# Kernel tuning notes

Hardware: AMD Instinct MI355X
Metric: run time of the kernel (lower is better)

Reference implementation:

```python
import jax, jax.numpy as jnp
import numpy as np

S = 2048          # sequence length == max_seq_len
B = 256           # input_bits per token
H = 8             # num voting heads
NPER = 12         # RAM bits per neuron: min(similarity_bits, 12)
NPOS = 11         # relative-position bits: ceil(log2(max_seq_len))
SIM = 2 * B + NPOS  # similarity input bits = [query | key | rel_dist]
THRESH = H // 2   # threshold aggregation cutoff
MAXD = S - 1


def setup_inputs() -> dict:
    key = jax.random.key(0)
    k1, k2, k3 = jax.random.split(key, 3)
    tokens = jax.random.randint(k1, (S, B), 0, 2).astype(jnp.int32)      # bit tokens
    conn = jax.random.randint(k2, (H, NPER), 0, SIM).astype(jnp.int32)   # RAM wiring per head
    table = jax.random.randint(k3, (H, 2 ** NPER), 0, 2).astype(jnp.int32)  # RAM contents (0/1)
    return {"tokens": tokens, "conn": conn, "table": table}


def reference(tokens, conn, table):
    powers = (1 << jnp.arange(NPER)).astype(jnp.int32)            # address bit weights
    q_mask = (conn < B).astype(jnp.int32)
    k_mask = ((conn >= B) & (conn < 2 * B)).astype(jnp.int32)
    p_mask = (conn >= 2 * B).astype(jnp.int32)

    # Address decomposes additively over the three concat regions since wiring is fixed.
    tq = jnp.take(tokens, jnp.clip(conn, 0, B - 1), axis=1)        # [S,H,NPER]
    q_contrib = jnp.sum(tq * (q_mask * powers)[None], axis=-1)     # [S,H]
    tk = jnp.take(tokens, jnp.clip(conn - B, 0, B - 1), axis=1)
    k_contrib = jnp.sum(tk * (k_mask * powers)[None], axis=-1)     # [S,H]

    d = jnp.arange(S)
    rel_bits = ((d[:, None] >> jnp.arange(NPOS)[None, :]) & 1).astype(jnp.int32)  # [S,NPOS]
    tp = jnp.take(rel_bits, jnp.clip(conn - 2 * B, 0, NPOS - 1), axis=1)          # [S,H,NPER]
    p_contrib = jnp.sum(tp * (p_mask * powers)[None], axis=-1)     # [S,H] indexed by distance

    i = jnp.arange(S)
    dist = jnp.clip(i[:, None] - i[None, :], 0, MAXD)              # [S,S]
    addr = q_contrib[:, None, :] + k_contrib[None, :, :] + p_contrib[dist]  # [S,S,H]
    head_bits = table[jnp.arange(H)[None, None, :], addr]          # [S,S,H] RAM lookups

    causal = i[None, :] <= i[:, None]
    votes = jnp.where(causal, head_bits.sum(-1), 0)                # [S,S]

    # threshold aggregation: XOR (per-bit parity) of tokens with vote >= THRESH
    include = (votes >= THRESH).astype(jnp.int32)                  # [S,S]
    parity = jnp.einsum('ij,jb->ib', include, tokens) % 2          # [S,B]
    # fallback: first token achieving the max vote when nothing clears threshold
    fallback = tokens[jnp.argmax(votes, axis=1)]                   # [S,B]
    any_included = include.sum(axis=1, keepdims=True) > 0
    out = jnp.where(any_included, parity, fallback)
    return out.astype(jnp.uint8)
```

## Files before the change

kernel.cpp:

```cpp
#include <hip/hip_runtime.h>
#include <stdint.h>

#define S 2048
#define B 256
#define THRESH 4

typedef unsigned long long u64;
typedef uint32_t u32;
typedef uint8_t u8;


__global__ void prep_kernel(const int* __restrict__ tokens,
                            const int* __restrict__ conn,
                            const int* __restrict__ table,
                            u64* __restrict__ ptok,
                            uint16_t* __restrict__ qc,
                            uint16_t* __restrict__ kc,
                            uint16_t* __restrict__ pc,
                            u8* __restrict__ tab8) {
    const int bi = blockIdx.x;
    const int tid = threadIdx.x;

    if (bi >= S) {
        const int base = (bi - S) * 1024 + tid * 4;
        const int4 v = *(const int4*)(table + base);
        uchar4 o;
        o.x = (u8)(v.x & 1); o.y = (u8)(v.y & 1);
        o.z = (u8)(v.z & 1); o.w = (u8)(v.w & 1);
        *(uchar4*)(tab8 + base) = o;
        return;
    }

    __shared__ u64 srow[4];
    const int i = bi;
    const int lane = tid & 63, wave = tid >> 6;

    const int t = tokens[i * B + tid];
    const u64 m = __ballot(t != 0);
    if (lane == 0) {
        srow[wave] = m;
        ptok[i * 4 + wave] = m;
    }
    __syncthreads();

    if (tid < 8) {
        const int h = tid;
        int q = 0, k = 0, p = 0;
        #pragma unroll
        for (int n = 0; n < 12; ++n) {
            const int c = conn[h * 12 + n];
            if (c < B) {
                q |= (int)((srow[c >> 6] >> (c & 63)) & 1) << n;
            } else if (c < 2 * B) {
                const int cc = c - B;
                k |= (int)((srow[cc >> 6] >> (cc & 63)) & 1) << n;
            } else {
                p |= ((i >> (c - 2 * B)) & 1) << n;
            }
        }
        qc[i * 8 + h] = (uint16_t)q;
        kc[i * 8 + h] = (uint16_t)k;
        pc[i * 8 + h] = (uint16_t)p;
    }
}

__device__ __forceinline__ int vote8(const u8* s_tab8, u64 a0, u64 a1) {
    const u32 lo0 = (u32)a0, hi0 = (u32)(a0 >> 32);
    const u32 lo1 = (u32)a1, hi1 = (u32)(a1 >> 32);
    int v;
    v  = s_tab8[          (lo0 & 0xFFF)];
    v += s_tab8[ 4096 + ((lo0 >> 16) & 0xFFF)];
    v += s_tab8[ 8192 +  (hi0 & 0xFFF)];
    v += s_tab8[12288 + ((hi0 >> 16) & 0xFFF)];
    v += s_tab8[16384 +  (lo1 & 0xFFF)];
    v += s_tab8[20480 + ((lo1 >> 16) & 0xFFF)];
    v += s_tab8[24576 +  (hi1 & 0xFFF)];
    v += s_tab8[28672 + ((hi1 >> 16) & 0xFFF)];
    return v;
}

__launch_bounds__(256)
__global__ void main_kernel(const u64* __restrict__ ptok,
                            const uint16_t* __restrict__ qc,
                            const uint16_t* __restrict__ kc,
                            const uint16_t* __restrict__ pc,
                            const u8* __restrict__ tab8,
                            int* __restrict__ out) {
    __shared__ u8  s_tab8[32768];
    __shared__ u64 s_part[8][256];
    __shared__ u64 s_p2[8][32];
    __shared__ u64 s_fin[8];
    __shared__ u64 s_kred[4];

    const int b   = blockIdx.x;
    const int tid = threadIdx.x;
    const int lane = tid & 63, wave = tid >> 6;

    #pragma unroll
    for (int k = 0; k < 8; ++k)
        ((uint4*)s_tab8)[tid + k * 256] = ((const uint4*)tab8)[tid + k * 256];
    __syncthreads();

    const int rowA = (b == 1023) ? 2047 : 2046 - b;
    const int rowB = (b == 1023) ? 1023 : b;
    const int nA    = rowA + 1;
    const int total = nA + rowB + 1;
    const int niter = total >> 9;

    const ulonglong2 qA = *(const ulonglong2*)(qc + rowA * 8);
    const ulonglong2 qB = *(const ulonglong2*)(qc + rowB * 8);

    u64 ax0=0, ax1=0, ax2=0, ax3=0;
    u64 bx0=0, bx1=0, bx2=0, bx3=0;
    u32 bkA = 2047u, bkB = 2047u;

    for (int it = 0; it < niter; ++it) {
        const int v0 = (it << 9) + tid;
        const int v1 = v0 + 256;

        const bool isA0 = (v0 < nA);
        const bool isA1 = (v1 < nA);
        const int j0 = isA0 ? v0 : v0 - nA;
        const int j1 = isA1 ? v1 : v1 - nA;
        const int d0 = (isA0 ? rowA : rowB) - j0;
        const int d1 = (isA1 ? rowA : rowB) - j1;

        const ulonglong2 kk0 = *(const ulonglong2*)(kc + j0 * 8);
        const ulonglong2 pp0 = *(const ulonglong2*)(pc + d0 * 8);
        const ulonglong2 t00 = *(const ulonglong2*)(ptok + j0 * 4);
        const ulonglong2 t01 = *(const ulonglong2*)(ptok + j0 * 4 + 2);
        const ulonglong2 kk1 = *(const ulonglong2*)(kc + j1 * 8);
        const ulonglong2 pp1 = *(const ulonglong2*)(pc + d1 * 8);
        const ulonglong2 t10 = *(const ulonglong2*)(ptok + j1 * 4);
        const ulonglong2 t11 = *(const ulonglong2*)(ptok + j1 * 4 + 2);

        const int vt0 = vote8(s_tab8, (isA0 ? qA.x : qB.x) + kk0.x + pp0.x,
                                      (isA0 ? qA.y : qB.y) + kk0.y + pp0.y);
        const int vt1 = vote8(s_tab8, (isA1 ? qA.x : qB.x) + kk1.x + pp1.x,
                                      (isA1 ? qA.y : qB.y) + kk1.y + pp1.y);

        const u32 vk0 = ((u32)(vt0 + 1) << 16) | (u32)(2047 - j0);
        const u32 vk1 = ((u32)(vt1 + 1) << 16) | (u32)(2047 - j1);

        if (isA0) { if (vk0 > bkA) bkA = vk0; } else { if (vk0 > bkB) bkB = vk0; }
        if (isA1) { if (vk1 > bkA) bkA = vk1; } else { if (vk1 > bkB) bkB = vk1; }

        if (vt0 >= THRESH) {
            if (isA0) { ax0 ^= t00.x; ax1 ^= t00.y; ax2 ^= t01.x; ax3 ^= t01.y; }
            else      { bx0 ^= t00.x; bx1 ^= t00.y; bx2 ^= t01.x; bx3 ^= t01.y; }
        }
        if (vt1 >= THRESH) {
            if (isA1) { ax0 ^= t10.x; ax1 ^= t10.y; ax2 ^= t11.x; ax3 ^= t11.y; }
            else      { bx0 ^= t10.x; bx1 ^= t10.y; bx2 ^= t11.x; bx3 ^= t11.y; }
        }
    }

    #pragma unroll
    for (int off = 32; off; off >>= 1) {
        bkA = max(bkA, (u32)__shfl_xor((int)bkA, off));
        bkB = max(bkB, (u32)__shfl_xor((int)bkB, off));
    }

    s_part[0][tid] = ax0; s_part[1][tid] = ax1; s_part[2][tid] = ax2; s_part[3][tid] = ax3;
    s_part[4][tid] = bx0; s_part[5][tid] = bx1; s_part[6][tid] = bx2; s_part[7][tid] = bx3;
    if (lane == 0) s_kred[wave] = ((u64)bkA << 32) | bkB;
    __syncthreads();

    {
        const int w = tid >> 5, c = tid & 31;
        u64 x = s_part[w][c]       ^ s_part[w][c + 32]  ^ s_part[w][c + 64]  ^ s_part[w][c + 96]
              ^ s_part[w][c + 128] ^ s_part[w][c + 160] ^ s_part[w][c + 192] ^ s_part[w][c + 224];
        s_p2[w][c] = x;
    }
    __syncthreads();
    if (tid < 64) {
        const int w = tid >> 3, c = tid & 7;
        u64 x = s_p2[w][c] ^ s_p2[w][c + 8] ^ s_p2[w][c + 16] ^ s_p2[w][c + 24];
        x ^= __shfl_xor(x, 4); x ^= __shfl_xor(x, 2); x ^= __shfl_xor(x, 1);
        if (c == 0) s_fin[w] = x;
    }
    __syncthreads();

    const u32 fkA = max(max((u32)(s_kred[0] >> 32), (u32)(s_kred[1] >> 32)),
                        max((u32)(s_kred[2] >> 32), (u32)(s_kred[3] >> 32)));
    const u32 fkB = max(max((u32)s_kred[0], (u32)s_kred[1]),
                        max((u32)s_kred[2], (u32)s_kred[3]));

    const int widx = tid >> 6, bitb = tid & 63;
    int oA, oB;
    if ((fkA >> 16) > THRESH) {
        oA = (int)((s_fin[widx] >> bitb) & 1);
    } else {
        const int bj = 2047 - (int)(fkA & 0xFFFF);
        oA = (int)((ptok[bj * 4 + widx] >> bitb) & 1);
    }
    if ((fkB >> 16) > THRESH) {
        oB = (int)((s_fin[4 + widx] >> bitb) & 1);
    } else {
        const int bj = 2047 - (int)(fkB & 0xFFFF);
        oB = (int)((ptok[bj * 4 + widx] >> bitb) & 1);
    }
    out[rowA * B + tid] = oA;
    out[rowB * B + tid] = oB;
}

extern "C" void kernel_launch(void* const* d_in, const int* in_sizes, int n_in,
                              void* d_out, int out_size, void* d_ws, size_t ws_size,
                              hipStream_t stream) {
    const int* tokens = (const int*)d_in[0];
    const int* conn   = (const int*)d_in[1];
    const int* table  = (const int*)d_in[2];
    int* outp = (int*)d_out;

    uint8_t* ws = (uint8_t*)d_ws;
    u64*      ptok = (u64*)(ws);
    uint16_t* qcp  = (uint16_t*)(ws + 65536);
    uint16_t* kcp  = (uint16_t*)(ws + 98304);
    uint16_t* pcp  = (uint16_t*)(ws + 131072);
    u8*       tab8 = (u8*)(ws + 163840);

    prep_kernel<<<S + 32, 256, 0, stream>>>(tokens, conn, table, ptok, qcp, kcp, pcp, tab8);
    main_kernel<<<S / 2, 256, 0, stream>>>(ptok, qcp, kcp, pcp, tab8, outp);
}
```

Before: 23.15 us.

## Bit-pack RAM tables into u32 words and batch 8 rows per prep block

Measured after the change: 19.83 us. 1.17x faster.

```diff
diff --git a/kernel.cpp b/kernel.cpp
--- a/kernel.cpp
+++ b/kernel.cpp
@@ -7,7 +7,6 @@
 
 typedef unsigned long long u64;
 typedef uint32_t u32;
-typedef uint8_t u8;
 
 
 __global__ void prep_kernel(const int* __restrict__ tokens,
@@ -17,43 +16,46 @@
                             uint16_t* __restrict__ qc,
                             uint16_t* __restrict__ kc,
                             uint16_t* __restrict__ pc,
-                            u8* __restrict__ tab8) {
-    const int bi = blockIdx.x;
-    const int tid = threadIdx.x;
-
-    if (bi >= S) {
-        const int base = (bi - S) * 1024 + tid * 4;
-        const int4 v = *(const int4*)(table + base);
-        uchar4 o;
-        o.x = (u8)(v.x & 1); o.y = (u8)(v.y & 1);
-        o.z = (u8)(v.z & 1); o.w = (u8)(v.w & 1);
-        *(uchar4*)(tab8 + base) = o;
+                            u32* __restrict__ ptab) {
+    const int bi = blockIdx.x, tid = threadIdx.x;
+
+    if (bi >= 256) {
+        const int m = (bi - 256) * 256 + tid;
+        const int* src = table + m * 32;
+        u32 v = 0;
+        #pragma unroll
+        for (int b = 0; b < 32; ++b) v |= (u32)(src[b] & 1) << b;
+        ptab[m] = v;
         return;
     }
 
-    __shared__ u64 srow[4];
-    const int i = bi;
+    __shared__ u32 s_conn[96];
+    __shared__ u64 s_row[8][4];
     const int lane = tid & 63, wave = tid >> 6;
 
-    const int t = tokens[i * B + tid];
-    const u64 m = __ballot(t != 0);
-    if (lane == 0) {
-        srow[wave] = m;
-        ptok[i * 4 + wave] = m;
-    }
-    __syncthreads();
-
-    if (tid < 8) {
-        const int h = tid;
+    if (tid < 96) s_conn[tid] = (u32)conn[tid];
+
+    const int r0 = bi * 8;
+    #pragma unroll
+    for (int r = 0; r < 8; ++r) {
+        const int t = tokens[(r0 + r) * B + tid];
+        const u64 m = __ballot(t != 0);
+        if (lane == 0) { s_row[r][wave] = m; ptok[(r0 + r) * 4 + wave] = m; }
+    }
+    __syncthreads();
+
+    if (tid < 64) {
+        const int r = tid >> 3, h = tid & 7;
+        const int i = r0 + r;
         int q = 0, k = 0, p = 0;
         #pragma unroll
         for (int n = 0; n < 12; ++n) {
-            const int c = conn[h * 12 + n];
+            const int c = (int)s_conn[h * 12 + n];
             if (c < B) {
-                q |= (int)((srow[c >> 6] >> (c & 63)) & 1) << n;
+                q |= (int)((s_row[r][c >> 6] >> (c & 63)) & 1) << n;
             } else if (c < 2 * B) {
                 const int cc = c - B;
-                k |= (int)((srow[cc >> 6] >> (cc & 63)) & 1) << n;
+                k |= (int)((s_row[r][cc >> 6] >> (cc & 63)) & 1) << n;
             } else {
                 p |= ((i >> (c - 2 * B)) & 1) << n;
             }
@@ -64,18 +66,15 @@
     }
 }
 
-__device__ __forceinline__ int vote8(const u8* s_tab8, u64 a0, u64 a1) {
-    const u32 lo0 = (u32)a0, hi0 = (u32)(a0 >> 32);
-    const u32 lo1 = (u32)a1, hi1 = (u32)(a1 >> 32);
-    int v;
-    v  = s_tab8[          (lo0 & 0xFFF)];
-    v += s_tab8[ 4096 + ((lo0 >> 16) & 0xFFF)];
-    v += s_tab8[ 8192 +  (hi0 & 0xFFF)];
-    v += s_tab8[12288 + ((hi0 >> 16) & 0xFFF)];
-    v += s_tab8[16384 +  (lo1 & 0xFFF)];
-    v += s_tab8[20480 + ((lo1 >> 16) & 0xFFF)];
-    v += s_tab8[24576 +  (hi1 & 0xFFF)];
-    v += s_tab8[28672 + ((hi1 >> 16) & 0xFFF)];
+__device__ __forceinline__ int vote8(const u32* s_tab, u64 a0, u64 a1) {
+    int v = 0;
+    #pragma unroll
+    for (int h = 0; h < 4; ++h) {
+        { u32 w = (u32)(a0 >> (16 * h + 5)) & 127;
+          v += (int)((s_tab[h * 128 + w] >> ((u32)(a0 >> (16 * h)) & 31)) & 1); }
+        { u32 w = (u32)(a1 >> (16 * h + 5)) & 127;
+          v += (int)((s_tab[(h + 4) * 128 + w] >> ((u32)(a1 >> (16 * h)) & 31)) & 1); }
+    }
     return v;
 }
 
@@ -84,9 +83,9 @@
                             const uint16_t* __restrict__ qc,
                             const uint16_t* __restrict__ kc,
                             const uint16_t* __restrict__ pc,
-                            const u8* __restrict__ tab8,
+                            const u32* __restrict__ ptab,
                             int* __restrict__ out) {
-    __shared__ u8  s_tab8[32768];
+    __shared__ u32 s_tab[1024];
     __shared__ u64 s_part[8][256];
     __shared__ u64 s_p2[8][32];
     __shared__ u64 s_fin[8];
@@ -96,9 +95,7 @@
     const int tid = threadIdx.x;
     const int lane = tid & 63, wave = tid >> 6;
 
-    #pragma unroll
-    for (int k = 0; k < 8; ++k)
-        ((uint4*)s_tab8)[tid + k * 256] = ((const uint4*)tab8)[tid + k * 256];
+    ((uint4*)s_tab)[tid] = ((const uint4*)ptab)[tid];
     __syncthreads();
 
     const int rowA = (b == 1023) ? 2047 : 2046 - b;
@@ -134,10 +131,10 @@
         const ulonglong2 t10 = *(const ulonglong2*)(ptok + j1 * 4);
         const ulonglong2 t11 = *(const ulonglong2*)(ptok + j1 * 4 + 2);
 
-        const int vt0 = vote8(s_tab8, (isA0 ? qA.x : qB.x) + kk0.x + pp0.x,
-                                      (isA0 ? qA.y : qB.y) + kk0.y + pp0.y);
-        const int vt1 = vote8(s_tab8, (isA1 ? qA.x : qB.x) + kk1.x + pp1.x,
-                                      (isA1 ? qA.y : qB.y) + kk1.y + pp1.y);
+        const int vt0 = vote8(s_tab, (isA0 ? qA.x : qB.x) + kk0.x + pp0.x,
+                                     (isA0 ? qA.y : qB.y) + kk0.y + pp0.y);
+        const int vt1 = vote8(s_tab, (isA1 ? qA.x : qB.x) + kk1.x + pp1.x,
+                                     (isA1 ? qA.y : qB.y) + kk1.y + pp1.y);
 
         const u32 vk0 = ((u32)(vt0 + 1) << 16) | (u32)(2047 - j0);
         const u32 vk1 = ((u32)(vt1 + 1) << 16) | (u32)(2047 - j1);
@@ -217,8 +214,8 @@
     uint16_t* qcp  = (uint16_t*)(ws + 65536);
     uint16_t* kcp  = (uint16_t*)(ws + 98304);
     uint16_t* pcp  = (uint16_t*)(ws + 131072);
-    u8*       tab8 = (u8*)(ws + 163840);
-
-    prep_kernel<<<S + 32, 256, 0, stream>>>(tokens, conn, table, ptok, qcp, kcp, pcp, tab8);
-    main_kernel<<<S / 2, 256, 0, stream>>>(ptok, qcp, kcp, pcp, tab8, outp);
-}
+    u32*      ptab = (u32*)(ws + 163840);
+
+    prep_kernel<<<260, 256, 0, stream>>>(tokens, conn, table, ptok, qcp, kcp, pcp, ptab);
+    main_kernel<<<S / 2, 256, 0, stream>>>(ptok, qcp, kcp, pcp, ptab, outp);
+}
```

## Batch prep rows per block and alias reduction buffer onto table LDS

Applied to the files above, without the earlier changes.

New measurement: 20.87 us. -9.9%, faster.

```diff
diff --git a/kernel.cpp b/kernel.cpp
--- a/kernel.cpp
+++ b/kernel.cpp
@@ -18,11 +18,10 @@
                             uint16_t* __restrict__ kc,
                             uint16_t* __restrict__ pc,
                             u8* __restrict__ tab8) {
-    const int bi = blockIdx.x;
-    const int tid = threadIdx.x;
-
-    if (bi >= S) {
-        const int base = (bi - S) * 1024 + tid * 4;
+    const int bi = blockIdx.x, tid = threadIdx.x;
+
+    if (bi >= 256) {
+        const int base = (bi - 256) * 1024 + tid * 4;
         const int4 v = *(const int4*)(table + base);
         uchar4 o;
         o.x = (u8)(v.x & 1); o.y = (u8)(v.y & 1);
@@ -31,29 +30,33 @@
         return;
     }
 
-    __shared__ u64 srow[4];
-    const int i = bi;
+    __shared__ u32 s_conn[96];
+    __shared__ u64 s_row[8][4];
     const int lane = tid & 63, wave = tid >> 6;
 
-    const int t = tokens[i * B + tid];
-    const u64 m = __ballot(t != 0);
-    if (lane == 0) {
-        srow[wave] = m;
-        ptok[i * 4 + wave] = m;
-    }
-    __syncthreads();
-
-    if (tid < 8) {
-        const int h = tid;
+    if (tid < 96) s_conn[tid] = (u32)conn[tid];
+
+    const int r0 = bi * 8;
+    #pragma unroll
+    for (int r = 0; r < 8; ++r) {
+        const int t = tokens[(r0 + r) * B + tid];
+        const u64 m = __ballot(t != 0);
+        if (lane == 0) { s_row[r][wave] = m; ptok[(r0 + r) * 4 + wave] = m; }
+    }
+    __syncthreads();
+
+    if (tid < 64) {
+        const int r = tid >> 3, h = tid & 7;
+        const int i = r0 + r;
         int q = 0, k = 0, p = 0;
         #pragma unroll
         for (int n = 0; n < 12; ++n) {
-            const int c = conn[h * 12 + n];
+            const int c = (int)s_conn[h * 12 + n];
             if (c < B) {
-                q |= (int)((srow[c >> 6] >> (c & 63)) & 1) << n;
+                q |= (int)((s_row[r][c >> 6] >> (c & 63)) & 1) << n;
             } else if (c < 2 * B) {
                 const int cc = c - B;
-                k |= (int)((srow[cc >> 6] >> (cc & 63)) & 1) << n;
+                k |= (int)((s_row[r][cc >> 6] >> (cc & 63)) & 1) << n;
             } else {
                 p |= ((i >> (c - 2 * B)) & 1) << n;
             }
@@ -86,11 +89,14 @@
                             const uint16_t* __restrict__ pc,
                             const u8* __restrict__ tab8,
                             int* __restrict__ out) {
-    __shared__ u8  s_tab8[32768];
-    __shared__ u64 s_part[8][256];
+    __shared__ __align__(16) u8 s_mem[32768];
     __shared__ u64 s_p2[8][32];
     __shared__ u64 s_fin[8];
     __shared__ u64 s_kred[4];
+
+    u8* s_tab8 = s_mem;
+    typedef u64 part_row[256];
+    part_row* s_part = reinterpret_cast<part_row*>(s_mem);
 
     const int b   = blockIdx.x;
     const int tid = threadIdx.x;
@@ -115,43 +121,28 @@
     u32 bkA = 2047u, bkB = 2047u;
 
     for (int it = 0; it < niter; ++it) {
-        const int v0 = (it << 9) + tid;
-        const int v1 = v0 + 256;
-
-        const bool isA0 = (v0 < nA);
-        const bool isA1 = (v1 < nA);
-        const int j0 = isA0 ? v0 : v0 - nA;
-        const int j1 = isA1 ? v1 : v1 - nA;
-        const int d0 = (isA0 ? rowA : rowB) - j0;
-        const int d1 = (isA1 ? rowA : rowB) - j1;
-
-        const ulonglong2 kk0 = *(const ulonglong2*)(kc + j0 * 8);
-        const ulonglong2 pp0 = *(const ulonglong2*)(pc + d0 * 8);
-        const ulonglong2 t00 = *(const ulonglong2*)(ptok + j0 * 4);
-        const ulonglong2 t01 = *(const ulonglong2*)(ptok + j0 * 4 + 2);
-        const ulonglong2 kk1 = *(const ulonglong2*)(kc + j1 * 8);
-        const ulonglong2 pp1 = *(const ulonglong2*)(pc + d1 * 8);
-        const ulonglong2 t10 = *(const ulonglong2*)(ptok + j1 * 4);
-        const ulonglong2 t11 = *(const ulonglong2*)(ptok + j1 * 4 + 2);
-
-        const int vt0 = vote8(s_tab8, (isA0 ? qA.x : qB.x) + kk0.x + pp0.x,
-                                      (isA0 ? qA.y : qB.y) + kk0.y + pp0.y);
-        const int vt1 = vote8(s_tab8, (isA1 ? qA.x : qB.x) + kk1.x + pp1.x,
-                                      (isA1 ? qA.y : qB.y) + kk1.y + pp1.y);
-
-        const u32 vk0 = ((u32)(vt0 + 1) << 16) | (u32)(2047 - j0);
-        const u32 vk1 = ((u32)(vt1 + 1) << 16) | (u32)(2047 - j1);
-
-        if (isA0) { if (vk0 > bkA) bkA = vk0; } else { if (vk0 > bkB) bkB = vk0; }
-        if (isA1) { if (vk1 > bkA) bkA = vk1; } else { if (vk1 > bkB) bkB = vk1; }
-
-        if (vt0 >= THRESH) {
-            if (isA0) { ax0 ^= t00.x; ax1 ^= t00.y; ax2 ^= t01.x; ax3 ^= t01.y; }
-            else      { bx0 ^= t00.x; bx1 ^= t00.y; bx2 ^= t01.x; bx3 ^= t01.y; }
-        }
-        if (vt1 >= THRESH) {
-            if (isA1) { ax0 ^= t10.x; ax1 ^= t10.y; ax2 ^= t11.x; ax3 ^= t11.y; }
-            else      { bx0 ^= t10.x; bx1 ^= t10.y; bx2 ^= t11.x; bx3 ^= t11.y; }
+        #pragma unroll
+        for (int s = 0; s < 2; ++s) {
+            const int v = (it << 9) + (s << 8) + tid;
+            const bool isA = (v < nA);
+            const int j = isA ? v : v - nA;
+            const int d = (isA ? rowA : rowB) - j;
+
+            const ulonglong2 kk = *(const ulonglong2*)(kc + j * 8);
+            const ulonglong2 pp = *(const ulonglong2*)(pc + d * 8);
+            const ulonglong2 t0 = *(const ulonglong2*)(ptok + j * 4);
+            const ulonglong2 t1 = *(const ulonglong2*)(ptok + j * 4 + 2);
+
+            const int vt = vote8(s_tab8, (isA ? qA.x : qB.x) + kk.x + pp.x,
+                                         (isA ? qA.y : qB.y) + kk.y + pp.y);
+
+            const u32 vk = ((u32)(vt + 1) << 16) | (u32)(2047 - j);
+            if (isA) { if (vk > bkA) bkA = vk; } else { if (vk > bkB) bkB = vk; }
+
+            if (vt >= THRESH) {
+                if (isA) { ax0 ^= t0.x; ax1 ^= t0.y; ax2 ^= t1.x; ax3 ^= t1.y; }
+                else     { bx0 ^= t0.x; bx1 ^= t0.y; bx2 ^= t1.x; bx3 ^= t1.y; }
+            }
         }
     }
 
@@ -161,6 +152,7 @@
         bkB = max(bkB, (u32)__shfl_xor((int)bkB, off));
     }
 
+    __syncthreads();
     s_part[0][tid] = ax0; s_part[1][tid] = ax1; s_part[2][tid] = ax2; s_part[3][tid] = ax3;
     s_part[4][tid] = bx0; s_part[5][tid] = bx1; s_part[6][tid] = bx2; s_part[7][tid] = bx3;
     if (lane == 0) s_kred[wave] = ((u64)bkA << 32) | bkB;
@@ -219,6 +211,6 @@
     uint16_t* pcp  = (uint16_t*)(ws + 131072);
     u8*       tab8 = (u8*)(ws + 163840);
 
-    prep_kernel<<<S + 32, 256, 0, stream>>>(tokens, conn, table, ptok, qcp, kcp, pcp, tab8);
+    prep_kernel<<<288, 256, 0, stream>>>(tokens, conn, table, ptok, qcp, kcp, pcp, tab8);
     main_kernel<<<S / 2, 256, 0, stream>>>(ptok, qcp, kcp, pcp, tab8, outp);
 }
```
